# Performance work log

Measured on AMD Instinct MI355X. Metric: run time of the kernel, lower is better.

The kernel has to match this reference:

```python
import jax, jax.numpy as jnp
import numpy as np

B, T, HID = 2, 2048, 2048
NH, DK, DV = 6, 256, 512
KEY_DIM, VAL_DIM = NH * DK, NH * DV
CONV = 4
EPS = 1e-5
SCALE = DK ** -0.5


def setup_inputs() -> dict:
    ks = jax.random.split(jax.random.key(0), 14)
    g = lambda k, shape, s=1.0: jax.random.normal(k, shape, jnp.float32) * s
    # dt_bias init as in the module: inv_dt = dt + log(-expm1(-dt))
    dt = jnp.exp(jax.random.uniform(ks[12], (NH,), jnp.float32)
                 * (np.log(0.1) - np.log(0.001)) + np.log(0.001))
    dt = jnp.clip(dt, 1e-4, None)
    inv_dt = dt + jnp.log(-jnp.expm1(-dt))
    return {
        "hidden_states": g(ks[0], (B, T, HID)),
        "w_q": g(ks[1], (HID, KEY_DIM), HID ** -0.5),
        "w_k": g(ks[2], (HID, KEY_DIM), HID ** -0.5),
        "w_v": g(ks[3], (HID, VAL_DIM), HID ** -0.5),
        "w_a": g(ks[4], (HID, NH), HID ** -0.5),
        "w_b": g(ks[5], (HID, NH), HID ** -0.5),
        "w_g": g(ks[6], (HID, VAL_DIM), HID ** -0.5),
        "w_o": g(ks[7], (VAL_DIM, HID), VAL_DIM ** -0.5),
        "conv_q": g(ks[8], (KEY_DIM, CONV), CONV ** -0.5),
        "conv_k": g(ks[9], (KEY_DIM, CONV), CONV ** -0.5),
        "conv_v": g(ks[10], (VAL_DIM, CONV), CONV ** -0.5),
        "A_log": jnp.log(jax.random.uniform(ks[11], (NH,), jnp.float32, 1e-3, 16.0)),
        "dt_bias": inv_dt,
        "norm_w": jnp.ones((DV,), jnp.float32),
    }


def short_conv(x, w):
    # depthwise causal conv1d, kernel size CONV, followed by SiLU
    K = w.shape[1]
    xp = jnp.pad(x, ((0, 0), (K - 1, 0), (0, 0)))  # left pad (causal)
    out = sum(xp[:, j:j + x.shape[1], :] * w[:, j] for j in range(K))
    return jax.nn.silu(out)


def l2norm(x):
    n = jnp.sqrt(jnp.sum(x * x, axis=-1, keepdims=True))
    return x / jnp.maximum(n, 1e-6)


def gated_delta_rule(q, k, v, glog, beta):
    # q,k: [B,T,H,DK]; v: [B,T,H,DV]; glog,beta: [B,T,H]
    # S_t = exp(g_t) (I - b_t k_t k_t^T) S_{t-1} + b_t k_t v_t^T ; o_t = scale * q_t^T S_t
    tm = lambda x: jnp.moveaxis(x, 1, 0)  # time-major

    def step(S, xs):  # S: [B,H,DK,DV]
        qt, kt, vt, gt, bt = xs
        Sd = jnp.exp(gt)[..., None, None] * S
        kS = jnp.einsum('bhk,bhkv->bhv', kt, Sd)           # k^T (a S)
        u = bt[..., None] * (vt - kS)                       # [B,H,DV]
        S_new = Sd + kt[..., None] * u[:, :, None, :]       # rank-1 update
        ot = SCALE * jnp.einsum('bhk,bhkv->bhv', qt, S_new)
        return S_new, ot

    S0 = jnp.zeros((B, NH, DK, DV), q.dtype)
    _, o = jax.lax.scan(step, S0, (tm(q), tm(k), tm(v), tm(glog), tm(beta)))
    return jnp.moveaxis(o, 0, 1)  # [B,T,H,DV]


def reference(hidden_states, w_q, w_k, w_v, w_a, w_b, w_g, w_o,
              conv_q, conv_k, conv_v, A_log, dt_bias, norm_w):
    x = hidden_states
    q = short_conv(x @ w_q, conv_q).reshape(B, T, NH, DK)
    k = short_conv(x @ w_k, conv_k).reshape(B, T, NH, DK)
    v = short_conv(x @ w_v, conv_v).reshape(B, T, NH, DV)
    beta = jax.nn.sigmoid(x @ w_b)                          # [B,T,H]
    glog = -jnp.exp(A_log) * jax.nn.softplus(x @ w_a + dt_bias)
    q = l2norm(q)
    k = l2norm(k)
    o = gated_delta_rule(q, k, v, glog, beta)               # [B,T,H,DV]
    # gated RMSNorm: rmsnorm(o) * w * silu(g_out)
    g_out = (x @ w_g).reshape(B, T, NH, DV)
    o = o * jax.lax.rsqrt(jnp.mean(o * o, axis=-1, keepdims=True) + EPS)
    o = o * norm_w * jax.nn.silu(g_out)
    return o.reshape(B, T, VAL_DIM) @ w_o
```

## Files before the change

### kernel.cpp

```cpp
#include <hip/hip_runtime.h>
#include <hip/hip_bf16.h>
#include <cstdint>

#define B_ 2
#define T_ 2048
#define HID 2048
#define NH 6
#define DK 256
#define DV 512
#define KEY_DIM (NH*DK)
#define VAL_DIM (NH*DV)
#define EPS_ 1e-5f
#define SCALE_ 0.0625f
#define MT (B_*T_)
#define CC 64
#define NC (T_/CC)

typedef __attribute__((ext_vector_type(8))) short short8;
typedef __attribute__((ext_vector_type(4))) float floatx4;
typedef __attribute__((ext_vector_type(4))) unsigned int uint4v;

union Pk8 { unsigned short us[8]; uint4v v; };

__device__ inline unsigned short f32_to_bf16(float f) {
    union { float f; unsigned int u; } v; v.f = f;
    unsigned int u = v.u;
    u += 0x7fffu + ((u >> 16) & 1u);
    return (unsigned short)(u >> 16);
}

__device__ inline float bf16_to_f32(unsigned short u) {
    union { unsigned int u; float f; } v; v.u = ((unsigned int)u) << 16;
    return v.f;
}

__device__ inline float silu_f(float x) { return x / (1.f + expf(-x)); }

__device__ inline void gl_lds16(const unsigned short* g, unsigned short* l) {
    __builtin_amdgcn_global_load_lds(
        (const __attribute__((address_space(1))) unsigned int*)g,
        (__attribute__((address_space(3))) unsigned int*)l, 16, 0, 0);
}

__global__ __launch_bounds__(256) void cvt_bf16_kernel(const float* __restrict__ in,
                                                       unsigned short* __restrict__ out, int n) {
    int i = (blockIdx.x * 256 + threadIdx.x) * 4;
    if (i >= n) return;
    float4 v = *reinterpret_cast<const float4*>(in + i);
    ushort4 o;
    o.x = f32_to_bf16(v.x); o.y = f32_to_bf16(v.y);
    o.z = f32_to_bf16(v.z); o.w = f32_to_bf16(v.w);
    *reinterpret_cast<ushort4*>(out + i) = o;
}

__global__ __launch_bounds__(256) void transpose_cvt_kernel(const float* __restrict__ in,
                                                            unsigned short* __restrict__ out,
                                                            int K, int N) {
    __shared__ float tile[64][65];
    int k0 = blockIdx.x * 64, n0 = blockIdx.y * 64;
    int r = threadIdx.x >> 2, c0 = (threadIdx.x & 3) * 16;
    const float* src = in + (size_t)(k0 + r) * N + n0 + c0;
#pragma unroll
    for (int j = 0; j < 16; j += 4) {
        float4 v = *reinterpret_cast<const float4*>(src + j);
        tile[r][c0 + j + 0] = v.x; tile[r][c0 + j + 1] = v.y;
        tile[r][c0 + j + 2] = v.z; tile[r][c0 + j + 3] = v.w;
    }
    __syncthreads();
    int n = threadIdx.x >> 2, kc = (threadIdx.x & 3) * 16;
    unsigned short* dst = out + (size_t)(n0 + n) * K + k0 + kc;
#pragma unroll
    for (int j = 0; j < 16; j += 4) {
        ushort4 o;
        o.x = f32_to_bf16(tile[kc + j + 0][n]);
        o.y = f32_to_bf16(tile[kc + j + 1][n]);
        o.z = f32_to_bf16(tile[kc + j + 2][n]);
        o.w = f32_to_bf16(tile[kc + j + 3][n]);
        *reinterpret_cast<ushort4*>(dst + j) = o;
    }
}

#define BM 128
#define BN 128
#define BK 32

__global__ __launch_bounds__(256) void gemm_bf16_kernel(const unsigned short* __restrict__ A,
                                                        const unsigned short* __restrict__ BT,
                                                        float* __restrict__ C,
                                                        int M, int N, int K) {
    __shared__ __align__(16) unsigned short As[BM * BK];
    __shared__ __align__(16) unsigned short Bs[BN * BK];
    int tid = threadIdx.x;
    int m0 = blockIdx.y * BM, n0 = blockIdx.x * BN;
    int wave = tid >> 6, lane = tid & 63;
    int wr = (wave >> 1) * 64, wc = (wave & 1) * 64;
    int l15 = lane & 15, lh = lane >> 4;

    int srow = wave * 16 + (lane >> 2);
    int scol = (lane & 3) * 8;
    const unsigned short* agp0 = A + (size_t)(m0 + srow) * K + scol;
    const unsigned short* agp1 = A + (size_t)(m0 + srow + 64) * K + scol;
    const unsigned short* bgp0 = BT + (size_t)(n0 + srow) * K + scol;
    const unsigned short* bgp1 = BT + (size_t)(n0 + srow + 64) * K + scol;
    unsigned short* asl0 = As + wave * 512;
    unsigned short* asl1 = As + 2048 + wave * 512;
    unsigned short* bsl0 = Bs + wave * 512;
    unsigned short* bsl1 = Bs + 2048 + wave * 512;

    floatx4 acc[4][4];
#pragma unroll
    for (int m = 0; m < 4; m++)
#pragma unroll
        for (int n = 0; n < 4; n++) acc[m][n] = (floatx4){0.f, 0.f, 0.f, 0.f};

    for (int kt = 0; kt < K; kt += BK) {
        __syncthreads();
        gl_lds16(agp0 + kt, asl0);
        gl_lds16(agp1 + kt, asl1);
        gl_lds16(bgp0 + kt, bsl0);
        gl_lds16(bgp1 + kt, bsl1);
        __syncthreads();
        short8 a[4], b[4];
#pragma unroll
        for (int i = 0; i < 4; i++)
            a[i] = *reinterpret_cast<const short8*>(As + (wr + i * 16 + l15) * BK + lh * 8);
#pragma unroll
        for (int i = 0; i < 4; i++)
            b[i] = *reinterpret_cast<const short8*>(Bs + (wc + i * 16 + l15) * BK + lh * 8);
#pragma unroll
        for (int m = 0; m < 4; m++)
#pragma unroll
            for (int n = 0; n < 4; n++)
                acc[m][n] = __builtin_amdgcn_mfma_f32_16x16x32_bf16(a[m], b[n], acc[m][n], 0, 0, 0);
    }

#pragma unroll
    for (int m = 0; m < 4; m++)
#pragma unroll
        for (int n = 0; n < 4; n++) {
            int row = m0 + wr + m * 16 + lh * 4;
            int col = n0 + wc + n * 16 + l15;
#pragma unroll
            for (int j = 0; j < 4; j++)
                C[(size_t)(row + j) * N + col] = acc[m][n][j];
        }
}

__global__ __launch_bounds__(256) void ab_kernel(const float* __restrict__ x,
                                                 const float* __restrict__ wa,
                                                 const float* __restrict__ wb,
                                                 const float* __restrict__ A_log,
                                                 const float* __restrict__ dtb,
                                                 float* __restrict__ glog,
                                                 float* __restrict__ beta) {
    int bt = blockIdx.x, tid = threadIdx.x;
    const float* xr = x + (size_t)bt * HID;
    float pa[NH], pb[NH];
#pragma unroll
    for (int h = 0; h < NH; h++) { pa[h] = 0.f; pb[h] = 0.f; }
    for (int k = tid; k < HID; k += 256) {
        float xv = xr[k];
#pragma unroll
        for (int h = 0; h < NH; h++) {
            pa[h] = fmaf(xv, wa[k * NH + h], pa[h]);
            pb[h] = fmaf(xv, wb[k * NH + h], pb[h]);
        }
    }
    __shared__ float red[256][12];
#pragma unroll
    for (int h = 0; h < NH; h++) { red[tid][h] = pa[h]; red[tid][NH + h] = pb[h]; }
    __syncthreads();
    for (int s = 128; s > 0; s >>= 1) {
        if (tid < s)
#pragma unroll
            for (int j = 0; j < 12; j++) red[tid][j] += red[tid + s][j];
        __syncthreads();
    }
    if (tid < NH) {
        float a = red[0][tid] + dtb[tid];
        float sp = (a > 20.f) ? a : log1pf(expf(a));
        glog[(size_t)bt * NH + tid] = -expf(A_log[tid]) * sp;
        float bv = red[0][NH + tid];
        beta[(size_t)bt * NH + tid] = 1.f / (1.f + expf(-bv));
    }
}

__global__ __launch_bounds__(256) void conv_silu_l2norm_kernel(const float* __restrict__ in,
                                                               const float* __restrict__ w,
                                                               float* __restrict__ out) {
    int bt = blockIdx.x;
    int h = blockIdx.y;
    int t = bt & (T_ - 1);
    int c = h * DK + threadIdx.x;
    float4 wv = *reinterpret_cast<const float4*>(w + (size_t)c * 4);
    float acc = 0.f;
    if (t >= 3) {
        acc = in[(size_t)(bt - 3) * KEY_DIM + c] * wv.x
            + in[(size_t)(bt - 2) * KEY_DIM + c] * wv.y
            + in[(size_t)(bt - 1) * KEY_DIM + c] * wv.z
            + in[(size_t)(bt) * KEY_DIM + c] * wv.w;
    } else {
        if (t - 3 >= 0) acc = fmaf(in[(size_t)(bt - 3) * KEY_DIM + c], wv.x, acc);
        if (t - 2 >= 0) acc = fmaf(in[(size_t)(bt - 2) * KEY_DIM + c], wv.y, acc);
        if (t - 1 >= 0) acc = fmaf(in[(size_t)(bt - 1) * KEY_DIM + c], wv.z, acc);
        acc = fmaf(in[(size_t)bt * KEY_DIM + c], wv.w, acc);
    }
    float s = silu_f(acc);
    float ss = s * s;
#pragma unroll
    for (int m = 1; m < 64; m <<= 1) ss += __shfl_xor(ss, m);
    __shared__ float wsum[4];
    if ((threadIdx.x & 63) == 0) wsum[threadIdx.x >> 6] = ss;
    __syncthreads();
    float tot = wsum[0] + wsum[1] + wsum[2] + wsum[3];
    float r = 1.f / fmaxf(sqrtf(tot), 1e-6f);
    out[(size_t)bt * KEY_DIM + c] = s * r;
}

__global__ __launch_bounds__(256) void conv_silu_kernel(const float* __restrict__ in,
                                                        const float* __restrict__ w,
                                                        float* __restrict__ out) {
    int bt = blockIdx.x;
    int c = blockIdx.y * 256 + threadIdx.x;
    int t = bt & (T_ - 1);
    float4 wv = *reinterpret_cast<const float4*>(w + (size_t)c * 4);
    float acc = 0.f;
    if (t >= 3) {
        acc = in[(size_t)(bt - 3) * VAL_DIM + c] * wv.x
            + in[(size_t)(bt - 2) * VAL_DIM + c] * wv.y
            + in[(size_t)(bt - 1) * VAL_DIM + c] * wv.z
            + in[(size_t)(bt) * VAL_DIM + c] * wv.w;
    } else {
        if (t - 3 >= 0) acc = fmaf(in[(size_t)(bt - 3) * VAL_DIM + c], wv.x, acc);
        if (t - 2 >= 0) acc = fmaf(in[(size_t)(bt - 2) * VAL_DIM + c], wv.y, acc);
        if (t - 1 >= 0) acc = fmaf(in[(size_t)(bt - 1) * VAL_DIM + c], wv.z, acc);
        acc = fmaf(in[(size_t)bt * VAL_DIM + c], wv.w, acc);
    }
    out[(size_t)bt * VAL_DIM + c] = silu_f(acc);
}

__global__ __launch_bounds__(256) void chunk_prep_kernel(
    const float* __restrict__ QC, const float* __restrict__ KC, const float* __restrict__ VC,
    const float* __restrict__ GL, const float* __restrict__ BE,
    unsigned short* __restrict__ Qg, unsigned short* __restrict__ KB,
    unsigned short* __restrict__ KlT, unsigned short* __restrict__ Tm,
    unsigned short* __restrict__ Am, unsigned short* __restrict__ BVT,
    float* __restrict__ gend) {
    int c = blockIdx.x;
    int bh = blockIdx.y;
    int b = bh / NH, h = bh % NH;
    size_t idx = (size_t)bh * NC + c;
    int bt0 = b * T_ + c * CC;

    __shared__ __align__(16) char ldsbuf[64 * 264 * 2 * 2];
    unsigned short* Kb = (unsigned short*)ldsbuf;
    unsigned short* Qb = (unsigned short*)(ldsbuf + 33792);
    float* Vst = (float*)ldsbuf;
    float* Msf = (float*)(ldsbuf + 33792);
    unsigned short* Ts_lds = (unsigned short*)(ldsbuf + 50432);
    __shared__ float gc[64], es[64], bb_s[64], gtmp[64];

    int tid = threadIdx.x, wave = tid >> 6, lane = tid & 63;
    int l15 = lane & 15, lh = lane >> 4;

    if (tid < 64) {
        gtmp[tid] = GL[(size_t)(bt0 + tid) * NH + h];
        bb_s[tid] = BE[(size_t)(bt0 + tid) * NH + h];
    }

    {
        int r = tid >> 2, seg = (tid & 3) * 64;
        const float* ksrc = KC + (size_t)(bt0 + r) * KEY_DIM + h * DK + seg;
        const float* qsrc = QC + (size_t)(bt0 + r) * KEY_DIM + h * DK + seg;
#pragma unroll
        for (int jj = 0; jj < 8; jj++) {
            float4 a = *reinterpret_cast<const float4*>(ksrc + jj * 8);
            float4 a2 = *reinterpret_cast<const float4*>(ksrc + jj * 8 + 4);
            Pk8 pk;
            pk.us[0] = f32_to_bf16(a.x);  pk.us[1] = f32_to_bf16(a.y);
            pk.us[2] = f32_to_bf16(a.z);  pk.us[3] = f32_to_bf16(a.w);
            pk.us[4] = f32_to_bf16(a2.x); pk.us[5] = f32_to_bf16(a2.y);
            pk.us[6] = f32_to_bf16(a2.z); pk.us[7] = f32_to_bf16(a2.w);
            *reinterpret_cast<uint4v*>(Kb + r * 264 + seg + jj * 8) = pk.v;
            float4 qa = *reinterpret_cast<const float4*>(qsrc + jj * 8);
            float4 qa2 = *reinterpret_cast<const float4*>(qsrc + jj * 8 + 4);
            pk.us[0] = f32_to_bf16(qa.x);  pk.us[1] = f32_to_bf16(qa.y);
            pk.us[2] = f32_to_bf16(qa.z);  pk.us[3] = f32_to_bf16(qa.w);
            pk.us[4] = f32_to_bf16(qa2.x); pk.us[5] = f32_to_bf16(qa2.y);
            pk.us[6] = f32_to_bf16(qa2.z); pk.us[7] = f32_to_bf16(qa2.w);
            *reinterpret_cast<uint4v*>(Qb + r * 264 + seg + jj * 8) = pk.v;
        }
    }
    __syncthreads();

    if (wave == 0) {
        float xg = gtmp[lane];
#pragma unroll
        for (int off = 1; off < 64; off <<= 1) {
            float yg = __shfl_up(xg, off, 64);
            if (lane >= off) xg += yg;
        }
        gc[lane] = xg;
    }

    floatx4 kkf[4], qkf[4];
#pragma unroll
    for (int nt = 0; nt < 4; nt++) { kkf[nt] = (floatx4){0,0,0,0}; qkf[nt] = (floatx4){0,0,0,0}; }
#pragma unroll
    for (int kk = 0; kk < 8; kk++) {
        short8 ak = *reinterpret_cast<const short8*>(Kb + (wave * 16 + l15) * 264 + kk * 32 + lh * 8);
        short8 aq = *reinterpret_cast<const short8*>(Qb + (wave * 16 + l15) * 264 + kk * 32 + lh * 8);
#pragma unroll
        for (int nt = 0; nt < 4; nt++) {
            short8 bk = *reinterpret_cast<const short8*>(Kb + (nt * 16 + l15) * 264 + kk * 32 + lh * 8);
            kkf[nt] = __builtin_amdgcn_mfma_f32_16x16x32_bf16(ak, bk, kkf[nt], 0, 0, 0);
            qkf[nt] = __builtin_amdgcn_mfma_f32_16x16x32_bf16(aq, bk, qkf[nt], 0, 0, 0);
        }
    }
    __syncthreads();

    {
        int r = tid >> 2, seg = (tid & 3) * 64;
        float gmm = __expf(gc[r]);
        float qs = SCALE_ * gmm, ksc = bb_s[r] * gmm;
#pragma unroll
        for (int jj = 0; jj < 8; jj++) {
            Pk8 qi, ki, qo, ko;
            qi.v = *reinterpret_cast<const uint4v*>(Qb + r * 264 + seg + jj * 8);
            ki.v = *reinterpret_cast<const uint4v*>(Kb + r * 264 + seg + jj * 8);
#pragma unroll
            for (int e = 0; e < 8; e++) {
                qo.us[e] = f32_to_bf16(bf16_to_f32(qi.us[e]) * qs);
                ko.us[e] = f32_to_bf16(bf16_to_f32(ki.us[e]) * ksc);
            }
            *reinterpret_cast<uint4v*>(Qg + idx * 16384 + r * 256 + seg + jj * 8) = qo.v;
            *reinterpret_cast<uint4v*>(KB + idx * 16384 + r * 256 + seg + jj * 8) = ko.v;
        }
    }
    if (tid < 64) es[tid] = __expf(gc[63] - gc[tid]);
    __syncthreads();

#pragma unroll
    for (int nt = 0; nt < 4; nt++)
#pragma unroll
        for (int j = 0; j < 4; j++) {
            int t2 = wave * 16 + lh * 4 + j;
            int s2 = nt * 16 + l15;
            float dec = (s2 <= t2) ? __expf(gc[t2] - gc[s2]) : 0.f;
            Msf[t2 * 65 + s2] = (s2 < t2) ? bb_s[t2] * dec * kkf[nt][j] : 0.f;
            float av = (s2 <= t2) ? SCALE_ * dec * qkf[nt][j] : 0.f;
            Am[idx * 4096 + t2 * 64 + s2] = f32_to_bf16(av);
        }
    __syncthreads();

    {
        int t = lane;
        float a[16];
#pragma unroll
        for (int j2 = 0; j2 < 16; j2++) a[j2] = 0.f;
        float mcur = Msf[t * 65 + 0];
        for (int s = 0; s < 63; s++) {
            float mnext = Msf[t * 65 + s + 1];
            float m = (t > s) ? mcur : 0.f;
#pragma unroll
            for (int j2 = 0; j2 < 16; j2++) {
                int jg = 4 * j2 + wave;
                if (jg < s) {
                    float ra = __int_as_float(
                        __builtin_amdgcn_readlane(__float_as_int(a[j2]), s));
                    a[j2] = fmaf(m, -ra, a[j2]);
                } else if (jg == s) {
                    a[j2] += m;
                }
            }
            mcur = mnext;
        }
#pragma unroll
        for (int j2 = 0; j2 < 16; j2++) {
            int jg = 4 * j2 + wave;
            float v = (t == jg) ? 1.f : ((jg < t) ? -a[j2] : 0.f);
            Ts_lds[t * 72 + jg] = f32_to_bf16(v);
        }
    }
    __syncthreads();

    {
        int rr = tid >> 2, sseg = (tid & 3) * 16;
        *reinterpret_cast<uint4v*>(Tm + idx * 4096 + rr * 64 + sseg) =
            *reinterpret_cast<const uint4v*>(Ts_lds + rr * 72 + sseg);
        *reinterpret_cast<uint4v*>(Tm + idx * 4096 + rr * 64 + sseg + 8) =
            *reinterpret_cast<const uint4v*>(Ts_lds + rr * 72 + sseg + 8);
    }
    {
        int dk = tid;
#pragma unroll
        for (int sb = 0; sb < 8; sb++) {
            Pk8 pk;
#pragma unroll
            for (int e = 0; e < 8; e++) {
                int s = sb * 8 + e;
                pk.us[e] = f32_to_bf16(bf16_to_f32(Kb[s * 264 + dk]) * es[s]);
            }
            *reinterpret_cast<uint4v*>(KlT + idx * 16384 + dk * 64 + sb * 8) = pk.v;
        }
    }
    for (int hv = 0; hv < 2; hv++) {
        __syncthreads();
        int r = tid >> 2, seg = (tid & 3) * 64;
        const float* vsrc = VC + (size_t)(bt0 + r) * VAL_DIM + h * DV + hv * 256 + seg;
#pragma unroll
        for (int jj = 0; jj < 16; jj++)
            *reinterpret_cast<float4*>(Vst + r * 264 + seg + jj * 4) =
                *reinterpret_cast<const float4*>(vsrc + jj * 4);
        __syncthreads();
#pragma unroll
        for (int sb = 0; sb < 8; sb++) {
            Pk8 pk;
#pragma unroll
            for (int e = 0; e < 8; e++) {
                int s = sb * 8 + e;
                pk.us[e] = f32_to_bf16(Vst[s * 264 + tid] * bb_s[s]);
            }
            *reinterpret_cast<uint4v*>(BVT + idx * 32768 + (size_t)(hv * 256 + tid) * 64 + sb * 8) = pk.v;
        }
    }
    if (tid == 0) gend[idx] = __expf(gc[63]);
}

__global__ __launch_bounds__(128, 1) void chunk_scan_kernel(
    const unsigned short* __restrict__ Qg, const unsigned short* __restrict__ KBp,
    const unsigned short* __restrict__ KlTp, const unsigned short* __restrict__ Tmp_,
    const unsigned short* __restrict__ Amp_, const unsigned short* __restrict__ BVTp,
    const float* __restrict__ gendp, float* __restrict__ O) {
    int slice = blockIdx.x;
    int bh = blockIdx.y;
    int b = bh / NH, h = bh % NH;
    int tid = threadIdx.x, wave = tid >> 6, lane = tid & 63;
    int l15 = lane & 15, lh = lane >> 4;
    int dvbase = slice * 32 + wave * 16;

    __shared__ __align__(16) unsigned short QgB[64 * 264];
    __shared__ __align__(16) unsigned short KBB[64 * 264];
    __shared__ __align__(16) unsigned short KlTB[256 * 72];
    __shared__ __align__(16) unsigned short SbT[2][16 * 264];
    __shared__ __align__(16) unsigned short Wb[2][16 * 72];
    __shared__ __align__(16) unsigned short Ub[2][16 * 72];
    __shared__ __align__(16) float Ost[2][64 * 20];

    unsigned short* sbt = SbT[wave];
    unsigned short* wb  = Wb[wave];
    unsigned short* ub  = Ub[wave];
    float* ost = Ost[wave];

    floatx4 st[16];
#pragma unroll
    for (int i = 0; i < 16; i++) st[i] = (floatx4){0.f, 0.f, 0.f, 0.f};
    for (int i = lane; i < 16 * 264; i += 64) sbt[i] = 0;

    int r = tid >> 1, seg = (tid & 1) * 128;
    size_t idx0 = (size_t)bh * NC;

    uint4v qv[16], kv[16], klv[16];
    {
        const unsigned short* qg = Qg + idx0 * 16384;
        const unsigned short* kb = KBp + idx0 * 16384;
        const unsigned short* kl = KlTp + idx0 * 16384;
#pragma unroll
        for (int j = 0; j < 16; j++) {
            qv[j] = *reinterpret_cast<const uint4v*>(qg + r * 256 + seg + j * 8);
            kv[j] = *reinterpret_cast<const uint4v*>(kb + r * 256 + seg + j * 8);
        }
#pragma unroll
        for (int j = 0; j < 8; j++) {
            klv[j]     = *reinterpret_cast<const uint4v*>(kl + tid * 64 + j * 8);
            klv[j + 8] = *reinterpret_cast<const uint4v*>(kl + (tid + 128) * 64 + j * 8);
        }
    }

    for (int c = 0; c < NC; c++) {
        size_t idx = idx0 + c;
        const unsigned short* tm = Tmp_ + idx * 4096;
        const unsigned short* am = Amp_ + idx * 4096;
        const unsigned short* bvt = BVTp + idx * 32768;
        float ge = gendp[idx];

        __syncthreads();
#pragma unroll
        for (int j = 0; j < 16; j++) {
            *reinterpret_cast<uint4v*>(QgB + r * 264 + seg + j * 8) = qv[j];
            *reinterpret_cast<uint4v*>(KBB + r * 264 + seg + j * 8) = kv[j];
        }
#pragma unroll
        for (int j = 0; j < 8; j++) {
            *reinterpret_cast<uint4v*>(KlTB + tid * 72 + j * 8) = klv[j];
            *reinterpret_cast<uint4v*>(KlTB + (tid + 128) * 72 + j * 8) = klv[j + 8];
        }
        __syncthreads();

        if (c + 1 < NC) {
            const unsigned short* qg2 = Qg + (idx + 1) * 16384;
            const unsigned short* kb2 = KBp + (idx + 1) * 16384;
            const unsigned short* kl2 = KlTp + (idx + 1) * 16384;
#pragma unroll
            for (int j = 0; j < 16; j++) {
                qv[j] = *reinterpret_cast<const uint4v*>(qg2 + r * 256 + seg + j * 8);
                kv[j] = *reinterpret_cast<const uint4v*>(kb2 + r * 256 + seg + j * 8);
            }
#pragma unroll
            for (int j = 0; j < 8; j++) {
                klv[j]     = *reinterpret_cast<const uint4v*>(kl2 + tid * 64 + j * 8);
                klv[j + 8] = *reinterpret_cast<const uint4v*>(kl2 + (tid + 128) * 64 + j * 8);
            }
        }

        short8 tfr[4][2], afr[4][2];
#pragma unroll
        for (int nt = 0; nt < 4; nt++)
#pragma unroll
            for (int kk = 0; kk < 2; kk++) {
                tfr[nt][kk] = *reinterpret_cast<const short8*>(tm + (nt * 16 + l15) * 64 + kk * 32 + lh * 8);
                afr[nt][kk] = *reinterpret_cast<const short8*>(am + (nt * 16 + l15) * 64 + kk * 32 + lh * 8);
            }
        float bvv[4][4];
#pragma unroll
        for (int nt = 0; nt < 4; nt++)
#pragma unroll
            for (int j = 0; j < 4; j++)
                bvv[nt][j] = bf16_to_f32(bvt[(size_t)(dvbase + lh * 4 + j) * 64 + nt * 16 + l15]);

        floatx4 x2f[4], x1f[4];
#pragma unroll
        for (int nt = 0; nt < 4; nt++) { x2f[nt] = (floatx4){0,0,0,0}; x1f[nt] = (floatx4){0,0,0,0}; }
#pragma unroll
        for (int kk = 0; kk < 8; kk++) {
            short8 af = *reinterpret_cast<const short8*>(sbt + l15 * 264 + kk * 32 + lh * 8);
#pragma unroll
            for (int nt = 0; nt < 4; nt++) {
                short8 bq = *reinterpret_cast<const short8*>(QgB + (nt * 16 + l15) * 264 + kk * 32 + lh * 8);
                short8 bk = *reinterpret_cast<const short8*>(KBB + (nt * 16 + l15) * 264 + kk * 32 + lh * 8);
                x2f[nt] = __builtin_amdgcn_mfma_f32_16x16x32_bf16(af, bq, x2f[nt], 0, 0, 0);
                x1f[nt] = __builtin_amdgcn_mfma_f32_16x16x32_bf16(af, bk, x1f[nt], 0, 0, 0);
            }
        }

#pragma unroll
        for (int nt = 0; nt < 4; nt++)
#pragma unroll
            for (int j = 0; j < 4; j++)
                wb[(lh * 4 + j) * 72 + nt * 16 + l15] = f32_to_bf16(bvv[nt][j] - x1f[nt][j]);

        floatx4 uf[4];
#pragma unroll
        for (int nt = 0; nt < 4; nt++) uf[nt] = (floatx4){0,0,0,0};
#pragma unroll
        for (int kk = 0; kk < 2; kk++) {
            short8 af = *reinterpret_cast<const short8*>(wb + l15 * 72 + kk * 32 + lh * 8);
#pragma unroll
            for (int nt = 0; nt < 4; nt++)
                uf[nt] = __builtin_amdgcn_mfma_f32_16x16x32_bf16(af, tfr[nt][kk], uf[nt], 0, 0, 0);
        }
#pragma unroll
        for (int nt = 0; nt < 4; nt++)
#pragma unroll
            for (int j = 0; j < 4; j++)
                ub[(lh * 4 + j) * 72 + nt * 16 + l15] = f32_to_bf16(uf[nt][j]);

#pragma unroll
        for (int i = 0; i < 16; i++) st[i] = st[i] * ge;
#pragma unroll
        for (int kk = 0; kk < 2; kk++) {
            short8 af = *reinterpret_cast<const short8*>(ub + l15 * 72 + kk * 32 + lh * 8);
#pragma unroll
            for (int dkt = 0; dkt < 16; dkt++) {
                short8 bf = *reinterpret_cast<const short8*>(KlTB + (dkt * 16 + l15) * 72 + kk * 32 + lh * 8);
                st[dkt] = __builtin_amdgcn_mfma_f32_16x16x32_bf16(af, bf, st[dkt], 0, 0, 0);
            }
        }
#pragma unroll
        for (int dkt = 0; dkt < 16; dkt++)
#pragma unroll
            for (int j = 0; j < 4; j++)
                sbt[(lh * 4 + j) * 264 + dkt * 16 + l15] = f32_to_bf16(st[dkt][j]);

#pragma unroll
        for (int kk = 0; kk < 2; kk++) {
            short8 af = *reinterpret_cast<const short8*>(ub + l15 * 72 + kk * 32 + lh * 8);
#pragma unroll
            for (int nt = 0; nt < 4; nt++)
                x2f[nt] = __builtin_amdgcn_mfma_f32_16x16x32_bf16(af, afr[nt][kk], x2f[nt], 0, 0, 0);
        }
#pragma unroll
        for (int nt = 0; nt < 4; nt++)
#pragma unroll
            for (int j = 0; j < 4; j++)
                ost[(nt * 16 + l15) * 20 + lh * 4 + j] = x2f[nt][j];
        {
            float4 o0 = *reinterpret_cast<const float4*>(ost + lane * 20);
            float4 o1 = *reinterpret_cast<const float4*>(ost + lane * 20 + 4);
            float4 o2 = *reinterpret_cast<const float4*>(ost + lane * 20 + 8);
            float4 o3 = *reinterpret_cast<const float4*>(ost + lane * 20 + 12);
            size_t ga = ((size_t)(b * T_ + c * CC + lane)) * VAL_DIM + h * DV + dvbase;
            *reinterpret_cast<float4*>(O + ga)      = o0;
            *reinterpret_cast<float4*>(O + ga + 4)  = o1;
            *reinterpret_cast<float4*>(O + ga + 8)  = o2;
            *reinterpret_cast<float4*>(O + ga + 12) = o3;
        }
    }
}

__global__ __launch_bounds__(256) void gated_norm_kernel(const float* __restrict__ o,
                                                         const float* __restrict__ g,
                                                         const float* __restrict__ nw,
                                                         unsigned short* __restrict__ out) {
    int bt = blockIdx.x, h = blockIdx.y, tid = threadIdx.x;
    const float* orow = o + (size_t)bt * VAL_DIM + h * DV;
    const float* grow = g + (size_t)bt * VAL_DIM + h * DV;
    float x0 = orow[tid], x1 = orow[tid + 256];
    float ss = x0 * x0 + x1 * x1;
#pragma unroll
    for (int m = 1; m < 64; m <<= 1) ss += __shfl_xor(ss, m);
    __shared__ float wsum[4];
    if ((tid & 63) == 0) wsum[tid >> 6] = ss;
    __syncthreads();
    float tot = wsum[0] + wsum[1] + wsum[2] + wsum[3];
    float r = rsqrtf(tot / (float)DV + EPS_);
    float o0 = x0 * r * nw[tid] * silu_f(grow[tid]);
    float o1 = x1 * r * nw[tid + 256] * silu_f(grow[tid + 256]);
    unsigned short* orow_o = out + (size_t)bt * VAL_DIM + h * DV;
    orow_o[tid] = f32_to_bf16(o0);
    orow_o[tid + 256] = f32_to_bf16(o1);
}

extern "C" void kernel_launch(void* const* d_in, const int* in_sizes, int n_in,
                              void* d_out, int out_size, void* d_ws, size_t ws_size,
                              hipStream_t stream) {
    const float* x     = (const float*)d_in[0];
    const float* w_q   = (const float*)d_in[1];
    const float* w_k   = (const float*)d_in[2];
    const float* w_v   = (const float*)d_in[3];
    const float* w_a   = (const float*)d_in[4];
    const float* w_b   = (const float*)d_in[5];
    const float* w_g   = (const float*)d_in[6];
    const float* w_o   = (const float*)d_in[7];
    const float* cq    = (const float*)d_in[8];
    const float* ck    = (const float*)d_in[9];
    const float* cv    = (const float*)d_in[10];
    const float* A_log = (const float*)d_in[11];
    const float* dtb   = (const float*)d_in[12];
    const float* nw    = (const float*)d_in[13];
    float* out = (float*)d_out;

    char* ws = (char*)d_ws;
    size_t off = 0;
    auto alloc = [&](size_t bytes) {
        char* p = ws + off;
        off += (bytes + 255) & ~(size_t)255;
        return p;
    };
    unsigned short* xb = (unsigned short*)alloc((size_t)MT * HID * 2);
    unsigned short* wT = (unsigned short*)alloc((size_t)VAL_DIM * HID * 2);
    float* P1 = (float*)alloc((size_t)MT * KEY_DIM * 4);
    float* QC = (float*)alloc((size_t)MT * KEY_DIM * 4);
    float* KC = (float*)alloc((size_t)MT * KEY_DIM * 4);
    float* P2 = (float*)alloc((size_t)MT * VAL_DIM * 4);
    float* VC = (float*)alloc((size_t)MT * VAL_DIM * 4);
    float* GL = (float*)alloc((size_t)MT * NH * 4);
    float* BE = (float*)alloc((size_t)MT * NH * 4);
    const int NCH = 12 * NC;
    unsigned short* KlT = (unsigned short*)alloc((size_t)NCH * 256 * 64 * 2);
    unsigned short* Tm  = (unsigned short*)alloc((size_t)NCH * 4096 * 2);
    unsigned short* Am  = (unsigned short*)alloc((size_t)NCH * 4096 * 2);
    unsigned short* BVT = (unsigned short*)alloc((size_t)NCH * 512 * 64 * 2);
    float* gend = (float*)alloc((size_t)NCH * 4);

    unsigned short* Qg = (unsigned short*)P1;
    unsigned short* KB = (unsigned short*)P1 + (size_t)NCH * 16384;
    float* OB = VC;
    unsigned short* ONB = (unsigned short*)P1;

    cvt_bf16_kernel<<<(MT * HID) / 1024, 256, 0, stream>>>(x, xb, MT * HID);

    transpose_cvt_kernel<<<dim3(HID / 64, KEY_DIM / 64), 256, 0, stream>>>(w_q, wT, HID, KEY_DIM);
    gemm_bf16_kernel<<<dim3(KEY_DIM / BN, MT / BM), 256, 0, stream>>>(xb, wT, P1, MT, KEY_DIM, HID);
    conv_silu_l2norm_kernel<<<dim3(MT, NH), 256, 0, stream>>>(P1, cq, QC);

    transpose_cvt_kernel<<<dim3(HID / 64, KEY_DIM / 64), 256, 0, stream>>>(w_k, wT, HID, KEY_DIM);
    gemm_bf16_kernel<<<dim3(KEY_DIM / BN, MT / BM), 256, 0, stream>>>(xb, wT, P1, MT, KEY_DIM, HID);
    conv_silu_l2norm_kernel<<<dim3(MT, NH), 256, 0, stream>>>(P1, ck, KC);

    transpose_cvt_kernel<<<dim3(HID / 64, VAL_DIM / 64), 256, 0, stream>>>(w_v, wT, HID, VAL_DIM);
    gemm_bf16_kernel<<<dim3(VAL_DIM / BN, MT / BM), 256, 0, stream>>>(xb, wT, P2, MT, VAL_DIM, HID);
    conv_silu_kernel<<<dim3(MT, VAL_DIM / 256), 256, 0, stream>>>(P2, cv, VC);

    transpose_cvt_kernel<<<dim3(HID / 64, VAL_DIM / 64), 256, 0, stream>>>(w_g, wT, HID, VAL_DIM);
    gemm_bf16_kernel<<<dim3(VAL_DIM / BN, MT / BM), 256, 0, stream>>>(xb, wT, P2, MT, VAL_DIM, HID);

    ab_kernel<<<MT, 256, 0, stream>>>(x, w_a, w_b, A_log, dtb, GL, BE);

    chunk_prep_kernel<<<dim3(NC, 12), 256, 0, stream>>>(QC, KC, VC, GL, BE,
                                                        Qg, KB, KlT, Tm, Am, BVT, gend);
    chunk_scan_kernel<<<dim3(16, 12), 128, 0, stream>>>(Qg, KB, KlT, Tm, Am, BVT, gend, OB);

    gated_norm_kernel<<<dim3(MT, NH), 256, 0, stream>>>(OB, P2, nw, ONB);

    transpose_cvt_kernel<<<dim3(VAL_DIM / 64, HID / 64), 256, 0, stream>>>(w_o, wT, VAL_DIM, HID);
    gemm_bf16_kernel<<<dim3(HID / BN, MT / BM), 256, 0, stream>>>(ONB, wT, out, MT, HID, VAL_DIM);
}
```

Measured before the change: 1.056 ms.

## Split chunk-scan work across 8 waves per block with shared state tiles

The chunk scan kernel goes from 2 waves (each owning a 16-column DV slice and the full DK state) to 8 waves per block. The work is split over a 2x4 grid of DV rows by time/DK columns, so each wave holds a quarter of the state in registers. This cuts per-wave register pressure and serial MFMA chains and shrinks the per-thread prefetch buffers. The block index is also remapped, with a stride of 24, to spread (b,h) slices across XCDs. In exchange it adds several block-wide __syncthreads per chunk to exchange W, U and the state through shared memory.

```diff
diff --git a/kernel.cpp b/kernel.cpp
--- a/kernel.cpp
+++ b/kernel.cpp
@@ -427,53 +427,50 @@
     if (tid == 0) gend[idx] = __expf(gc[63]);
 }
 
-__global__ __launch_bounds__(128, 1) void chunk_scan_kernel(
+__global__ __launch_bounds__(512, 1) void chunk_scan_kernel(
     const unsigned short* __restrict__ Qg, const unsigned short* __restrict__ KBp,
     const unsigned short* __restrict__ KlTp, const unsigned short* __restrict__ Tmp_,
     const unsigned short* __restrict__ Amp_, const unsigned short* __restrict__ BVTp,
     const float* __restrict__ gendp, float* __restrict__ O) {
-    int slice = blockIdx.x;
-    int bh = blockIdx.y;
+    int bid = blockIdx.x;
+    int xs = bid & 7, js = bid >> 3;
+    int L = xs * 24 + js;
+    int bh = L >> 4, slice = L & 15;
     int b = bh / NH, h = bh % NH;
+    int dvbase = slice * 32;
     int tid = threadIdx.x, wave = tid >> 6, lane = tid & 63;
     int l15 = lane & 15, lh = lane >> 4;
-    int dvbase = slice * 32 + wave * 16;
+    int ms = wave >> 2;
+    int ns = wave & 3;
+    int tb = ns * 16;
 
     __shared__ __align__(16) unsigned short QgB[64 * 264];
     __shared__ __align__(16) unsigned short KBB[64 * 264];
     __shared__ __align__(16) unsigned short KlTB[256 * 72];
-    __shared__ __align__(16) unsigned short SbT[2][16 * 264];
-    __shared__ __align__(16) unsigned short Wb[2][16 * 72];
-    __shared__ __align__(16) unsigned short Ub[2][16 * 72];
-    __shared__ __align__(16) float Ost[2][64 * 20];
-
-    unsigned short* sbt = SbT[wave];
-    unsigned short* wb  = Wb[wave];
-    unsigned short* ub  = Ub[wave];
-    float* ost = Ost[wave];
-
-    floatx4 st[16];
-#pragma unroll
-    for (int i = 0; i < 16; i++) st[i] = (floatx4){0.f, 0.f, 0.f, 0.f};
-    for (int i = lane; i < 16 * 264; i += 64) sbt[i] = 0;
-
-    int r = tid >> 1, seg = (tid & 1) * 128;
+    __shared__ __align__(16) unsigned short SbT[32 * 264];
+    __shared__ __align__(16) unsigned short Wb[32 * 72];
+    __shared__ __align__(16) unsigned short Ub[32 * 72];
+    __shared__ __align__(16) float Ost[64 * 36];
+
+    floatx4 st[4];
+#pragma unroll
+    for (int i = 0; i < 4; i++) st[i] = (floatx4){0.f, 0.f, 0.f, 0.f};
+    for (int i = tid; i < 32 * 264; i += 512) SbT[i] = 0;
+
+    int sr = tid >> 3, sseg = (tid & 7) * 32;
+    int kr = tid >> 1, kseg = (tid & 1) * 32;
     size_t idx0 = (size_t)bh * NC;
 
-    uint4v qv[16], kv[16], klv[16];
+    uint4v qv[4], kv[4], klv[4];
     {
-        const unsigned short* qg = Qg + idx0 * 16384;
-        const unsigned short* kb = KBp + idx0 * 16384;
-        const unsigned short* kl = KlTp + idx0 * 16384;
-#pragma unroll
-        for (int j = 0; j < 16; j++) {
-            qv[j] = *reinterpret_cast<const uint4v*>(qg + r * 256 + seg + j * 8);
-            kv[j] = *reinterpret_cast<const uint4v*>(kb + r * 256 + seg + j * 8);
-        }
-#pragma unroll
-        for (int j = 0; j < 8; j++) {
-            klv[j]     = *reinterpret_cast<const uint4v*>(kl + tid * 64 + j * 8);
-            klv[j + 8] = *reinterpret_cast<const uint4v*>(kl + (tid + 128) * 64 + j * 8);
+        const unsigned short* qg0 = Qg + idx0 * 16384;
+        const unsigned short* kb0 = KBp + idx0 * 16384;
+        const unsigned short* kl0 = KlTp + idx0 * 16384;
+#pragma unroll
+        for (int j = 0; j < 4; j++) {
+            qv[j] = *reinterpret_cast<const uint4v*>(qg0 + sr * 256 + sseg + j * 8);
+            kv[j] = *reinterpret_cast<const uint4v*>(kb0 + sr * 256 + sseg + j * 8);
+            klv[j] = *reinterpret_cast<const uint4v*>(kl0 + kr * 64 + kseg + j * 8);
         }
     }
 
@@ -486,14 +483,10 @@
 
         __syncthreads();
 #pragma unroll
-        for (int j = 0; j < 16; j++) {
-            *reinterpret_cast<uint4v*>(QgB + r * 264 + seg + j * 8) = qv[j];
-            *reinterpret_cast<uint4v*>(KBB + r * 264 + seg + j * 8) = kv[j];
-        }
-#pragma unroll
-        for (int j = 0; j < 8; j++) {
-            *reinterpret_cast<uint4v*>(KlTB + tid * 72 + j * 8) = klv[j];
-            *reinterpret_cast<uint4v*>(KlTB + (tid + 128) * 72 + j * 8) = klv[j + 8];
+        for (int j = 0; j < 4; j++) {
+            *reinterpret_cast<uint4v*>(QgB + sr * 264 + sseg + j * 8) = qv[j];
+            *reinterpret_cast<uint4v*>(KBB + sr * 264 + sseg + j * 8) = kv[j];
+            *reinterpret_cast<uint4v*>(KlTB + kr * 72 + kseg + j * 8) = klv[j];
         }
         __syncthreads();
 
@@ -502,108 +495,81 @@
             const unsigned short* kb2 = KBp + (idx + 1) * 16384;
             const unsigned short* kl2 = KlTp + (idx + 1) * 16384;
 #pragma unroll
-            for (int j = 0; j < 16; j++) {
-                qv[j] = *reinterpret_cast<const uint4v*>(qg2 + r * 256 + seg + j * 8);
-                kv[j] = *reinterpret_cast<const uint4v*>(kb2 + r * 256 + seg + j * 8);
+            for (int j = 0; j < 4; j++) {
+                qv[j] = *reinterpret_cast<const uint4v*>(qg2 + sr * 256 + sseg + j * 8);
+                kv[j] = *reinterpret_cast<const uint4v*>(kb2 + sr * 256 + sseg + j * 8);
+                klv[j] = *reinterpret_cast<const uint4v*>(kl2 + kr * 64 + kseg + j * 8);
             }
-#pragma unroll
-            for (int j = 0; j < 8; j++) {
-                klv[j]     = *reinterpret_cast<const uint4v*>(kl2 + tid * 64 + j * 8);
-                klv[j + 8] = *reinterpret_cast<const uint4v*>(kl2 + (tid + 128) * 64 + j * 8);
-            }
-        }
-
-        short8 tfr[4][2], afr[4][2];
-#pragma unroll
-        for (int nt = 0; nt < 4; nt++)
-#pragma unroll
-            for (int kk = 0; kk < 2; kk++) {
-                tfr[nt][kk] = *reinterpret_cast<const short8*>(tm + (nt * 16 + l15) * 64 + kk * 32 + lh * 8);
-                afr[nt][kk] = *reinterpret_cast<const short8*>(am + (nt * 16 + l15) * 64 + kk * 32 + lh * 8);
-            }
-        float bvv[4][4];
-#pragma unroll
-        for (int nt = 0; nt < 4; nt++)
-#pragma unroll
-            for (int j = 0; j < 4; j++)
-                bvv[nt][j] = bf16_to_f32(bvt[(size_t)(dvbase + lh * 4 + j) * 64 + nt * 16 + l15]);
-
-        floatx4 x2f[4], x1f[4];
-#pragma unroll
-        for (int nt = 0; nt < 4; nt++) { x2f[nt] = (floatx4){0,0,0,0}; x1f[nt] = (floatx4){0,0,0,0}; }
+        }
+
+        short8 tfr[2], afr[2];
+#pragma unroll
+        for (int kk = 0; kk < 2; kk++) {
+            tfr[kk] = *reinterpret_cast<const short8*>(tm + (tb + l15) * 64 + kk * 32 + lh * 8);
+            afr[kk] = *reinterpret_cast<const short8*>(am + (tb + l15) * 64 + kk * 32 + lh * 8);
+        }
+        float bvv[4];
+#pragma unroll
+        for (int j = 0; j < 4; j++)
+            bvv[j] = bf16_to_f32(bvt[(size_t)(dvbase + ms * 16 + lh * 4 + j) * 64 + tb + l15]);
+
+        floatx4 x2f = (floatx4){0,0,0,0}, x1f = (floatx4){0,0,0,0};
 #pragma unroll
         for (int kk = 0; kk < 8; kk++) {
-            short8 af = *reinterpret_cast<const short8*>(sbt + l15 * 264 + kk * 32 + lh * 8);
-#pragma unroll
-            for (int nt = 0; nt < 4; nt++) {
-                short8 bq = *reinterpret_cast<const short8*>(QgB + (nt * 16 + l15) * 264 + kk * 32 + lh * 8);
-                short8 bk = *reinterpret_cast<const short8*>(KBB + (nt * 16 + l15) * 264 + kk * 32 + lh * 8);
-                x2f[nt] = __builtin_amdgcn_mfma_f32_16x16x32_bf16(af, bq, x2f[nt], 0, 0, 0);
-                x1f[nt] = __builtin_amdgcn_mfma_f32_16x16x32_bf16(af, bk, x1f[nt], 0, 0, 0);
-            }
-        }
-
-#pragma unroll
-        for (int nt = 0; nt < 4; nt++)
-#pragma unroll
-            for (int j = 0; j < 4; j++)
-                wb[(lh * 4 + j) * 72 + nt * 16 + l15] = f32_to_bf16(bvv[nt][j] - x1f[nt][j]);
-
-        floatx4 uf[4];
-#pragma unroll
-        for (int nt = 0; nt < 4; nt++) uf[nt] = (floatx4){0,0,0,0};
+            short8 af = *reinterpret_cast<const short8*>(SbT + (ms * 16 + l15) * 264 + kk * 32 + lh * 8);
+            short8 bq = *reinterpret_cast<const short8*>(QgB + (tb + l15) * 264 + kk * 32 + lh * 8);
+            short8 bk = *reinterpret_cast<const short8*>(KBB + (tb + l15) * 264 + kk * 32 + lh * 8);
+            x2f = __builtin_amdgcn_mfma_f32_16x16x32_bf16(af, bq, x2f, 0, 0, 0);
+            x1f = __builtin_amdgcn_mfma_f32_16x16x32_bf16(af, bk, x1f, 0, 0, 0);
+        }
+#pragma unroll
+        for (int j = 0; j < 4; j++)
+            Wb[(ms * 16 + lh * 4 + j) * 72 + tb + l15] = f32_to_bf16(bvv[j] - x1f[j]);
+        __syncthreads();
+
+        floatx4 uf = (floatx4){0,0,0,0};
 #pragma unroll
         for (int kk = 0; kk < 2; kk++) {
-            short8 af = *reinterpret_cast<const short8*>(wb + l15 * 72 + kk * 32 + lh * 8);
-#pragma unroll
-            for (int nt = 0; nt < 4; nt++)
-                uf[nt] = __builtin_amdgcn_mfma_f32_16x16x32_bf16(af, tfr[nt][kk], uf[nt], 0, 0, 0);
-        }
-#pragma unroll
-        for (int nt = 0; nt < 4; nt++)
-#pragma unroll
-            for (int j = 0; j < 4; j++)
-                ub[(lh * 4 + j) * 72 + nt * 16 + l15] = f32_to_bf16(uf[nt][j]);
-
-#pragma unroll
-        for (int i = 0; i < 16; i++) st[i] = st[i] * ge;
+            short8 af = *reinterpret_cast<const short8*>(Wb + (ms * 16 + l15) * 72 + kk * 32 + lh * 8);
+            uf = __builtin_amdgcn_mfma_f32_16x16x32_bf16(af, tfr[kk], uf, 0, 0, 0);
+        }
+#pragma unroll
+        for (int j = 0; j < 4; j++)
+            Ub[(ms * 16 + lh * 4 + j) * 72 + tb + l15] = f32_to_bf16(uf[j]);
+        __syncthreads();
+
+#pragma unroll
+        for (int i = 0; i < 4; i++) st[i] = st[i] * ge;
 #pragma unroll
         for (int kk = 0; kk < 2; kk++) {
-            short8 af = *reinterpret_cast<const short8*>(ub + l15 * 72 + kk * 32 + lh * 8);
-#pragma unroll
-            for (int dkt = 0; dkt < 16; dkt++) {
-                short8 bf = *reinterpret_cast<const short8*>(KlTB + (dkt * 16 + l15) * 72 + kk * 32 + lh * 8);
+            short8 af = *reinterpret_cast<const short8*>(Ub + (ms * 16 + l15) * 72 + kk * 32 + lh * 8);
+#pragma unroll
+            for (int dkt = 0; dkt < 4; dkt++) {
+                short8 bf = *reinterpret_cast<const short8*>(KlTB + (ns * 64 + dkt * 16 + l15) * 72 + kk * 32 + lh * 8);
                 st[dkt] = __builtin_amdgcn_mfma_f32_16x16x32_bf16(af, bf, st[dkt], 0, 0, 0);
             }
         }
 #pragma unroll
-        for (int dkt = 0; dkt < 16; dkt++)
+        for (int dkt = 0; dkt < 4; dkt++)
 #pragma unroll
             for (int j = 0; j < 4; j++)
-                sbt[(lh * 4 + j) * 264 + dkt * 16 + l15] = f32_to_bf16(st[dkt][j]);
+                SbT[(ms * 16 + lh * 4 + j) * 264 + ns * 64 + dkt * 16 + l15] = f32_to_bf16(st[dkt][j]);
 
 #pragma unroll
         for (int kk = 0; kk < 2; kk++) {
-            short8 af = *reinterpret_cast<const short8*>(ub + l15 * 72 + kk * 32 + lh * 8);
-#pragma unroll
-            for (int nt = 0; nt < 4; nt++)
-                x2f[nt] = __builtin_amdgcn_mfma_f32_16x16x32_bf16(af, afr[nt][kk], x2f[nt], 0, 0, 0);
-        }
-#pragma unroll
-        for (int nt = 0; nt < 4; nt++)
-#pragma unroll
-            for (int j = 0; j < 4; j++)
-                ost[(nt * 16 + l15) * 20 + lh * 4 + j] = x2f[nt][j];
+            short8 af = *reinterpret_cast<const short8*>(Ub + (ms * 16 + l15) * 72 + kk * 32 + lh * 8);
+            x2f = __builtin_amdgcn_mfma_f32_16x16x32_bf16(af, afr[kk], x2f, 0, 0, 0);
+        }
+#pragma unroll
+        for (int j = 0; j < 4; j++)
+            Ost[(tb + l15) * 36 + ms * 16 + lh * 4 + j] = x2f[j];
+        __syncthreads();
+
         {
-            float4 o0 = *reinterpret_cast<const float4*>(ost + lane * 20);
-            float4 o1 = *reinterpret_cast<const float4*>(ost + lane * 20 + 4);
-            float4 o2 = *reinterpret_cast<const float4*>(ost + lane * 20 + 8);
-            float4 o3 = *reinterpret_cast<const float4*>(ost + lane * 20 + 12);
-            size_t ga = ((size_t)(b * T_ + c * CC + lane)) * VAL_DIM + h * DV + dvbase;
-            *reinterpret_cast<float4*>(O + ga)      = o0;
-            *reinterpret_cast<float4*>(O + ga + 4)  = o1;
-            *reinterpret_cast<float4*>(O + ga + 8)  = o2;
-            *reinterpret_cast<float4*>(O + ga + 12) = o3;
+            int tr = tid >> 3, dvs = (tid & 7) * 4;
+            float4 ov = *reinterpret_cast<const float4*>(Ost + tr * 36 + dvs);
+            size_t ga = ((size_t)(b * T_ + c * CC + tr)) * VAL_DIM + h * DV + dvbase + dvs;
+            *reinterpret_cast<float4*>(O + ga) = ov;
         }
     }
 }
@@ -699,7 +665,7 @@
 
     chunk_prep_kernel<<<dim3(NC, 12), 256, 0, stream>>>(QC, KC, VC, GL, BE,
                                                         Qg, KB, KlT, Tm, Am, BVT, gend);
-    chunk_scan_kernel<<<dim3(16, 12), 128, 0, stream>>>(Qg, KB, KlT, Tm, Am, BVT, gend, OB);
+    chunk_scan_kernel<<<192, 512, 0, stream>>>(Qg, KB, KlT, Tm, Am, BVT, gend, OB);
 
     gated_norm_kernel<<<dim3(MT, NH), 256, 0, stream>>>(OB, P2, nw, ONB);
 
```

Result: faster. 896.4 us (-15.1%).
